# Optimization experiments

Measured on AMD Instinct MI355X. Metric: run time of the kernel, lower is better.

Reference implementation:

```python
import math
import jax, jax.numpy as jnp
import numpy as np

B, L, D, K = 4, 8192, 256, 2
J = math.ceil(math.log((L - 1) / (K - 1) + 1) / math.log(K))  # 13


def setup_inputs() -> dict:
    key = jax.random.key(0)
    ks = jax.random.split(key, 6)
    h_scale = math.sqrt((math.gamma(K / 2) / math.gamma(J + K / 2)) ** (1.0 / J) / 2)
    return {
        "x": jax.random.normal(ks[0], (B, L, D), dtype=jnp.float32),
        "rms_scale": jnp.ones((D,), dtype=jnp.float32),
        "h0": h_scale * jax.random.normal(ks[1], (D, K), dtype=jnp.float32),
        "h1": h_scale * jax.random.normal(ks[2], (D, K), dtype=jnp.float32),
        "w": (1.0 / math.sqrt(J + 2)) * jax.random.normal(ks[3], (J + 2, D), dtype=jnp.float32),
        "conv_w": jax.random.normal(ks[4], (D, 2 * D), dtype=jnp.float32) / math.sqrt(D),
        "conv_b": jnp.zeros((2 * D,), dtype=jnp.float32),
    }


def _dw_conv(a, h, dilation, d):
    # depthwise dilated 1D conv, VALID padding; a: [B, Lpad, D], h: [1, D, K]
    return jax.lax.conv_general_dilated(
        lhs=a, rhs=h, window_strides=(1,), padding='VALID',
        dimension_numbers=('NLC', 'IOL', 'NLC'),
        rhs_dilation=(dilation,), feature_group_count=d)


def reference(x, rms_scale, h0, h1, w, conv_w, conv_b):
    d = x.shape[-1]
    k = h0.shape[-1]
    n_levels = w.shape[0] - 2
    skip = x
    # RMSNorm (flax default eps=1e-6)
    x = x * jax.lax.rsqrt(jnp.mean(jnp.square(x), axis=-1, keepdims=True) + 1e-6) * rms_scale
    # MultiResLayer (pad_right=False -> left pad, causal)
    h0e = h0[None, :, :]  # [1, D, K]
    h1e = h1[None, :, :]
    y = jnp.zeros_like(x)
    a = x
    for j in range(n_levels):
        dilation = k ** j
        pad = dilation * (k - 1)
        a = jnp.pad(a, ((0, 0), (pad, 0), (0, 0)))
        b = _dw_conv(a, h1e, dilation, d)
        a = _dw_conv(a, h0e, dilation, d)
        y = y + w[j + 1][None, None, :] * b
    y = y + w[None, :1, :] * x + w[None, -1:, :] * a
    # activation -> pointwise conv to 2D -> GLU -> residual
    y = jax.nn.gelu(y)  # approximate=True matches flax nn.gelu default
    y = jnp.einsum('bld,de->ble', y, conv_w) + conv_b
    y = jax.nn.glu(y, axis=-1)
    return y + skip
```

## Files before the change

kernel.cpp:

```cpp
#include <hip/hip_runtime.h>
#include <hip/hip_bf16.h>

#define B_ 4
#define L_ 8192
#define D_ 256
#define J_ 13

typedef __attribute__((ext_vector_type(4))) float f32x4;
typedef __attribute__((ext_vector_type(8))) short bf16x8;

__device__ __forceinline__ void async_copy16(const void* g, void* l) {
    __builtin_amdgcn_global_load_lds(
        (const __attribute__((address_space(1))) void*)g,
        (__attribute__((address_space(3))) void*)l, 16, 0, 0);
}

__global__ void wt_kernel(const float* __restrict__ W, __hip_bfloat16* __restrict__ Wt) {
    __shared__ float tile[64][65];
    int blk = blockIdx.x;
    int dt = blk >> 3, et = blk & 7;
    int d0 = dt * 64, e0 = et * 64;
    int tid = threadIdx.x;
#pragma unroll
    for (int k = 0; k < 16; ++k) {
        int i = tid + k * 256;
        int r = i >> 6, c = i & 63;
        tile[r][c] = W[(d0 + r) * 512 + e0 + c];
    }
    __syncthreads();
#pragma unroll
    for (int k = 0; k < 16; ++k) {
        int i = tid + k * 256;
        int r = i >> 6, c = i & 63;
        Wt[(e0 + r) * 256 + d0 + c] = __float2bfloat16(tile[c][r]);
    }
}

__global__ void rms_kernel(const float* __restrict__ x, const float* __restrict__ scale,
                           float* __restrict__ xt) {
    __shared__ float tile[32][257];
    __shared__ float invl[32];
    int blk = blockIdx.x;
    int b  = blk >> 8;
    int l0 = (blk & 255) << 5;
    int tid = threadIdx.x;
    const float* src = x + ((size_t)(b * L_ + l0)) * D_;
#pragma unroll
    for (int k = 0; k < 32; ++k) tile[k][tid] = src[k * D_ + tid];
    __syncthreads();
    int wave = tid >> 6, lane = tid & 63;
#pragma unroll
    for (int rr = 0; rr < 8; ++rr) {
        int r = wave * 8 + rr;
        float s = 0.f;
#pragma unroll
        for (int q = 0; q < 4; ++q) { float v = tile[r][lane + 64 * q]; s += v * v; }
#pragma unroll
        for (int off = 32; off; off >>= 1) s += __shfl_xor(s, off);
        if (lane == 0) invl[r] = rsqrtf(s * (1.0f / 256.0f) + 1e-6f);
    }
    __syncthreads();
#pragma unroll
    for (int k = 0; k < 32; ++k) {
        int i = tid + k * 256;
        int d = i >> 5, lr = i & 31;
        float v = tile[lr][d] * invl[lr] * scale[d];
        xt[((size_t)(b * D_ + d)) * L_ + l0 + lr] = v;
    }
}

__global__ void __launch_bounds__(512, 4) cascade_kernel(
    const float* __restrict__ xt, const float* __restrict__ h0,
    const float* __restrict__ h1, const float* __restrict__ w,
    __hip_bfloat16* __restrict__ ygt) {
    __shared__ float bufA[L_];
    __shared__ float bufB[L_];
    int blk = blockIdx.x;
    int c = blk & 255;
    int tid = threadIdx.x;
    const float4* s4 = (const float4*)(xt + ((size_t)blk) * L_);
    float4* a4 = (float4*)bufA;
#pragma unroll
    for (int q = 0; q < 4; ++q) a4[tid + q * 512] = s4[tid + q * 512];
    float h00 = h0[c * 2], h01 = h0[c * 2 + 1];
    float h10 = h1[c * 2], h11 = h1[c * 2 + 1];
    float w0 = w[c], wlast = w[14 * D_ + c];
    __syncthreads();

    float2 y[8];
    {
        float wj = w[1 * D_ + c];
        const float2* c2 = (const float2*)bufA;
        float2* n2 = (float2*)bufB;
#pragma unroll
        for (int m = 0; m < 8; ++m) {
            int p = tid + m * 512;
            float2 cv = c2[p];
            float px = (p > 0) ? bufA[2 * p - 1] : 0.f;
            float py = cv.x;
            y[m].x = w0 * cv.x + wj * (h10 * px + h11 * cv.x);
            y[m].y = w0 * cv.y + wj * (h10 * py + h11 * cv.y);
            n2[p] = make_float2(h00 * px + h01 * cv.x, h00 * py + h01 * cv.y);
        }
        __syncthreads();
    }
    float* cur = bufB;
    float* nxt = bufA;
#pragma unroll 1
    for (int j = 1; j < J_; ++j) {
        int dh = 1 << (j - 1);
        float wj = w[(j + 1) * D_ + c];
        const float2* c2 = (const float2*)cur;
        float2* n2 = (float2*)nxt;
#pragma unroll
        for (int m = 0; m < 8; ++m) {
            int p = tid + m * 512;
            float2 cv = c2[p];
            int q = p - dh;
            float2 pv = (q >= 0) ? c2[q] : make_float2(0.f, 0.f);
            y[m].x += wj * (h10 * pv.x + h11 * cv.x);
            y[m].y += wj * (h10 * pv.y + h11 * cv.y);
            n2[p] = make_float2(h00 * pv.x + h01 * cv.x, h00 * pv.y + h01 * cv.y);
        }
        __syncthreads();
        float* t = cur; cur = nxt; nxt = t;
    }
    {
        const float2* c2 = (const float2*)cur;
        __hip_bfloat162* o2 = (__hip_bfloat162*)(ygt + ((size_t)blk) * L_);
#pragma unroll
        for (int m = 0; m < 8; ++m) {
            int p = tid + m * 512;
            float2 cv = c2[p];
            float vx = y[m].x + wlast * cv.x;
            float vy = y[m].y + wlast * cv.y;
            float ux = 0.7978845608028654f * (vx + 0.044715f * vx * vx * vx);
            float uy = 0.7978845608028654f * (vy + 0.044715f * vy * vy * vy);
            float gx = 0.5f * vx * (1.f + tanhf(ux));
            float gy = 0.5f * vy * (1.f + tanhf(uy));
            __hip_bfloat162 o;
            o.x = __float2bfloat16(gx);
            o.y = __float2bfloat16(gy);
            o2[p] = o;
        }
    }
}

__global__ void trans_kernel(const ushort* __restrict__ ygt, ushort* __restrict__ yg) {
    __shared__ uint tile[64][33];
    int blk = blockIdx.x;
    int b = blk >> 9;
    int rem = blk & 511;
    int dt = rem >> 7, lt = rem & 127;
    int d0 = dt * 64, l0 = lt * 64;
    int tid = threadIdx.x;
    const uint* src = (const uint*)ygt;
#pragma unroll
    for (int k = 0; k < 8; ++k) {
        int i = tid + k * 256;
        int r = i >> 5, cp = i & 31;
        tile[r][cp] = src[(((size_t)(b * D_ + d0 + r)) * L_ + l0) / 2 + cp];
    }
    __syncthreads();
    const ushort* ts = (const ushort*)tile;
#pragma unroll
    for (int k = 0; k < 16; ++k) {
        int i = tid + k * 256;
        int r2 = i >> 6, c2 = i & 63;
        yg[((size_t)(b * L_ + l0 + r2)) * D_ + d0 + c2] = ts[c2 * 66 + r2];
    }
}

__global__ void __launch_bounds__(256) gemm_kernel(
    const ushort* __restrict__ yg, const ushort* __restrict__ Wt,
    const float* __restrict__ cb, const float* __restrict__ x,
    float* __restrict__ out) {
    __shared__ __align__(16) char smem[32768];
    ushort* As = (ushort*)smem;
    ushort* Bs = As + 128 * 64;
    int blk = blockIdx.x;
    int b = blk >> 8;
    int rem = blk & 255;
    int ltile = rem >> 2, et = rem & 3;
    int l0 = ltile * 128, e0 = et * 64;
    int tid = threadIdx.x;
    int wave = tid >> 6, lane = tid & 63;
    int wm = wave >> 1, wn = wave & 1;
    int m0 = wm * 64;

    int srow_in = (lane >> 3);
    int sg = lane & 7;
    int sgg = sg ^ srow_in;
    f32x4 acc[4][4];
#pragma unroll
    for (int i = 0; i < 4; ++i)
#pragma unroll
        for (int j = 0; j < 4; ++j) acc[i][j] = (f32x4)0.f;

    for (int kc = 0; kc < 4; ++kc) {
        __syncthreads();
#pragma unroll
        for (int v = 0; v < 4; ++v) {
            int r = wave * 32 + v * 8 + srow_in;
            async_copy16(yg + ((size_t)(b * L_ + l0 + r)) * D_ + kc * 64 + sgg * 8,
                         As + r * 64 + sg * 8);
            int e = (r < 64) ? (e0 + r) : (256 + e0 + (r - 64));
            async_copy16(Wt + e * 256 + kc * 64 + sgg * 8,
                         Bs + r * 64 + sg * 8);
        }
        __syncthreads();
#pragma unroll
        for (int kk = 0; kk < 2; ++kk) {
            bf16x8 af[4], bfr[4];
            int g = kk * 4 + (lane >> 4);
            int gp = (g ^ (lane & 7)) * 8;
#pragma unroll
            for (int mt = 0; mt < 4; ++mt)
                af[mt] = *(const bf16x8*)(As + (m0 + mt * 16 + (lane & 15)) * 64 + gp);
#pragma unroll
            for (int nt = 0; nt < 4; ++nt) {
                int n = wn * 32 + (nt & 1) * 16 + (nt >> 1) * 64 + (lane & 15);
                bfr[nt] = *(const bf16x8*)(Bs + n * 64 + gp);
            }
#pragma unroll
            for (int mt = 0; mt < 4; ++mt)
#pragma unroll
                for (int nt = 0; nt < 4; ++nt)
                    acc[mt][nt] = __builtin_amdgcn_mfma_f32_16x16x32_bf16(
                        af[mt], bfr[nt], acc[mt][nt], 0, 0, 0);
        }
    }
    __syncthreads();
    float* epi = (float*)smem;
    int row_in = (lane >> 4) * 4;
    int col = lane & 15;
#pragma unroll
    for (int mt = 0; mt < 4; ++mt) {
#pragma unroll
        for (int p = 0; p < 2; ++p) {
            f32x4 uacc = acc[mt][p];
            f32x4 vacc = acc[mt][p + 2];
            int ee = wn * 32 + p * 16 + col;
            float bu = cb[e0 + ee], bv = cb[256 + e0 + ee];
#pragma unroll
            for (int r = 0; r < 4; ++r) {
                int ll = m0 + mt * 16 + row_in + r;
                float u = uacc[r] + bu;
                float v = vacc[r] + bv;
                float g = u / (1.f + __expf(-v));
                epi[ll * 64 + (ee ^ ((ll & 4) ? 16 : 0))] = g;
            }
        }
    }
    __syncthreads();
#pragma unroll
    for (int k = 0; k < 8; ++k) {
        int i = tid + k * 256;
        int ll = i >> 4, e4 = i & 15;
        int ex = (e4 * 4) ^ ((ll & 4) ? 16 : 0);
        float4 gv = *(const float4*)(epi + ll * 64 + ex);
        size_t gidx = ((size_t)(b * L_ + l0 + ll)) * D_ + e0 + e4 * 4;
        float4 xv = *(const float4*)(x + gidx);
        float4 ov;
        ov.x = gv.x + xv.x; ov.y = gv.y + xv.y;
        ov.z = gv.z + xv.z; ov.w = gv.w + xv.w;
        *(float4*)(out + gidx) = ov;
    }
}

extern "C" void kernel_launch(void* const* d_in, const int* in_sizes, int n_in,
                              void* d_out, int out_size, void* d_ws, size_t ws_size,
                              hipStream_t stream) {
    const float* x  = (const float*)d_in[0];
    const float* rs = (const float*)d_in[1];
    const float* h0 = (const float*)d_in[2];
    const float* h1 = (const float*)d_in[3];
    const float* w  = (const float*)d_in[4];
    const float* cw = (const float*)d_in[5];
    const float* cb = (const float*)d_in[6];
    float* out = (float*)d_out;
    char* ws = (char*)d_ws;

    float*          xt  = (float*)ws;
    __hip_bfloat16* ygt = (__hip_bfloat16*)(ws + 33554432);
    __hip_bfloat16* Wt  = (__hip_bfloat16*)(ws + 50331648);
    ushort*         yg  = (ushort*)ws;

    wt_kernel<<<32, 256, 0, stream>>>(cw, Wt);
    rms_kernel<<<1024, 256, 0, stream>>>(x, rs, xt);
    cascade_kernel<<<1024, 512, 0, stream>>>(xt, h0, h1, w, ygt);
    trans_kernel<<<2048, 256, 0, stream>>>((const ushort*)ygt, yg);
    gemm_kernel<<<1024, 256, 0, stream>>>(yg, (const ushort*)Wt, cb, x, out);
}
```

Before: 163.9 us.

## Keep cascade state in registers with per-thread contiguous chunks and halo exchange

The dilated-conv cascade kernel now gives each thread 16 contiguous sequence elements held in registers, instead of ping-ponging full-length rows between two shared-memory buffers. The first four levels (dilation 1 to 8) read only the previous thread's tail through a small shared exchange buffer. Deeper levels shift whole thread chunks by exchanging them through shared memory. This cuts LDS traffic and size, so launch bounds rise to 6 blocks per CU for occupancy, but it adds an extra barrier per small level and more register pressure.

```diff
diff --git a/kernel.cpp b/kernel.cpp
--- a/kernel.cpp
+++ b/kernel.cpp
@@ -8,6 +8,7 @@
 
 typedef __attribute__((ext_vector_type(4))) float f32x4;
 typedef __attribute__((ext_vector_type(8))) short bf16x8;
+typedef __attribute__((ext_vector_type(8))) unsigned short u16x8;
 
 __device__ __forceinline__ void async_copy16(const void* g, void* l) {
     __builtin_amdgcn_global_load_lds(
@@ -69,81 +70,107 @@
     }
 }
 
-__global__ void __launch_bounds__(512, 4) cascade_kernel(
+#define LEVEL_SMALL(dconst)                                                     \
+    do {                                                                        \
+        *(float4*)&ex[t20 + 8]  = make_float4(cc[8], cc[9], cc[10], cc[11]);    \
+        *(float4*)&ex[t20 + 12] = make_float4(cc[12], cc[13], cc[14], cc[15]);  \
+        __syncthreads();                                                        \
+        float pt[8];                                                            \
+        if (t > 0) {                                                            \
+            float4 p0 = *(const float4*)&ex[t20 - 20 + 8];                      \
+            float4 p1 = *(const float4*)&ex[t20 - 20 + 12];                     \
+            pt[0]=p0.x; pt[1]=p0.y; pt[2]=p0.z; pt[3]=p0.w;                     \
+            pt[4]=p1.x; pt[5]=p1.y; pt[6]=p1.z; pt[7]=p1.w;                     \
+        } else { _Pragma("unroll") for (int i=0;i<8;++i) pt[i]=0.f; }           \
+        __syncthreads();                                                        \
+        float wj = w[((dconst##_J)+1) * D_ + c];                                \
+        _Pragma("unroll")                                                       \
+        for (int i = 15; i >= 0; --i) {                                         \
+            float pv = (i >= (dconst)) ? cc[i - (dconst)] : pt[8 + i - (dconst)]; \
+            float nv = h00 * pv + h01 * cc[i];                                  \
+            y[i] += wj * (h10 * pv + h11 * cc[i]);                              \
+            cc[i] = nv;                                                         \
+        }                                                                       \
+    } while (0)
+#define d1_J 0
+#define d2_J 1
+#define d4_J 2
+#define d8_J 3
+#define d1 1
+#define d2 2
+#define d4 4
+#define d8 8
+
+__global__ void __launch_bounds__(512, 6) cascade_kernel(
     const float* __restrict__ xt, const float* __restrict__ h0,
     const float* __restrict__ h1, const float* __restrict__ w,
     __hip_bfloat16* __restrict__ ygt) {
-    __shared__ float bufA[L_];
-    __shared__ float bufB[L_];
+    __shared__ float ex[512 * 20];
     int blk = blockIdx.x;
     int c = blk & 255;
-    int tid = threadIdx.x;
-    const float4* s4 = (const float4*)(xt + ((size_t)blk) * L_);
-    float4* a4 = (float4*)bufA;
-#pragma unroll
-    for (int q = 0; q < 4; ++q) a4[tid + q * 512] = s4[tid + q * 512];
+    int t = threadIdx.x;
+    int t20 = t * 20;
     float h00 = h0[c * 2], h01 = h0[c * 2 + 1];
     float h10 = h1[c * 2], h11 = h1[c * 2 + 1];
     float w0 = w[c], wlast = w[14 * D_ + c];
-    __syncthreads();
-
-    float2 y[8];
-    {
-        float wj = w[1 * D_ + c];
-        const float2* c2 = (const float2*)bufA;
-        float2* n2 = (float2*)bufB;
-#pragma unroll
-        for (int m = 0; m < 8; ++m) {
-            int p = tid + m * 512;
-            float2 cv = c2[p];
-            float px = (p > 0) ? bufA[2 * p - 1] : 0.f;
-            float py = cv.x;
-            y[m].x = w0 * cv.x + wj * (h10 * px + h11 * cv.x);
-            y[m].y = w0 * cv.y + wj * (h10 * py + h11 * cv.y);
-            n2[p] = make_float2(h00 * px + h01 * cv.x, h00 * py + h01 * cv.y);
-        }
+
+    const float* src = xt + ((size_t)blk) * L_ + t * 16;
+    float cc[16], y[16];
+#pragma unroll
+    for (int m = 0; m < 4; ++m) {
+        float4 v = *(const float4*)(src + 4 * m);
+        cc[4*m+0] = v.x; cc[4*m+1] = v.y; cc[4*m+2] = v.z; cc[4*m+3] = v.w;
+    }
+#pragma unroll
+    for (int i = 0; i < 16; ++i) y[i] = w0 * cc[i];
+
+    LEVEL_SMALL(d1);
+    LEVEL_SMALL(d2);
+    LEVEL_SMALL(d4);
+    LEVEL_SMALL(d8);
+
+#pragma unroll 1
+    for (int j = 4; j < J_; ++j) {
+        int dT = 1 << (j - 4);
+        float wj = w[(j + 1) * D_ + c];
+        *(float4*)&ex[t20 + 0]  = make_float4(cc[0], cc[1], cc[2], cc[3]);
+        *(float4*)&ex[t20 + 4]  = make_float4(cc[4], cc[5], cc[6], cc[7]);
+        *(float4*)&ex[t20 + 8]  = make_float4(cc[8], cc[9], cc[10], cc[11]);
+        *(float4*)&ex[t20 + 12] = make_float4(cc[12], cc[13], cc[14], cc[15]);
         __syncthreads();
-    }
-    float* cur = bufB;
-    float* nxt = bufA;
-#pragma unroll 1
-    for (int j = 1; j < J_; ++j) {
-        int dh = 1 << (j - 1);
-        float wj = w[(j + 1) * D_ + c];
-        const float2* c2 = (const float2*)cur;
-        float2* n2 = (float2*)nxt;
-#pragma unroll
-        for (int m = 0; m < 8; ++m) {
-            int p = tid + m * 512;
-            float2 cv = c2[p];
-            int q = p - dh;
-            float2 pv = (q >= 0) ? c2[q] : make_float2(0.f, 0.f);
-            y[m].x += wj * (h10 * pv.x + h11 * cv.x);
-            y[m].y += wj * (h10 * pv.y + h11 * cv.y);
-            n2[p] = make_float2(h00 * pv.x + h01 * cv.x, h00 * pv.y + h01 * cv.y);
+        float pv[16];
+        if (t >= dT) {
+            int pb = (t - dT) * 20;
+#pragma unroll
+            for (int m = 0; m < 4; ++m) {
+                float4 p = *(const float4*)&ex[pb + 4 * m];
+                pv[4*m+0] = p.x; pv[4*m+1] = p.y; pv[4*m+2] = p.z; pv[4*m+3] = p.w;
+            }
+        } else {
+#pragma unroll
+            for (int i = 0; i < 16; ++i) pv[i] = 0.f;
         }
         __syncthreads();
-        float* t = cur; cur = nxt; nxt = t;
-    }
-    {
-        const float2* c2 = (const float2*)cur;
-        __hip_bfloat162* o2 = (__hip_bfloat162*)(ygt + ((size_t)blk) * L_);
-#pragma unroll
-        for (int m = 0; m < 8; ++m) {
-            int p = tid + m * 512;
-            float2 cv = c2[p];
-            float vx = y[m].x + wlast * cv.x;
-            float vy = y[m].y + wlast * cv.y;
-            float ux = 0.7978845608028654f * (vx + 0.044715f * vx * vx * vx);
-            float uy = 0.7978845608028654f * (vy + 0.044715f * vy * vy * vy);
-            float gx = 0.5f * vx * (1.f + tanhf(ux));
-            float gy = 0.5f * vy * (1.f + tanhf(uy));
-            __hip_bfloat162 o;
-            o.x = __float2bfloat16(gx);
-            o.y = __float2bfloat16(gy);
-            o2[p] = o;
-        }
-    }
+#pragma unroll
+        for (int i = 0; i < 16; ++i) {
+            float nv = h00 * pv[i] + h01 * cc[i];
+            y[i] += wj * (h10 * pv[i] + h11 * cc[i]);
+            cc[i] = nv;
+        }
+    }
+    u16x8 o0, o1;
+#pragma unroll
+    for (int i = 0; i < 16; ++i) {
+        float v = y[i] + wlast * cc[i];
+        float u = 0.7978845608028654f * (v + 0.044715f * v * v * v);
+        float g = 0.5f * v * (1.f + tanhf(u));
+        union { __hip_bfloat16 b; unsigned short us; } cvt;
+        cvt.b = __float2bfloat16(g);
+        if (i < 8) o0[i] = cvt.us; else o1[i - 8] = cvt.us;
+    }
+    unsigned short* dst = (unsigned short*)(ygt + ((size_t)blk) * L_ + t * 16);
+    *(u16x8*)dst = o0;
+    *(u16x8*)(dst + 8) = o1;
 }
 
 __global__ void trans_kernel(const ushort* __restrict__ ygt, ushort* __restrict__ yg) {
```

Result: slower. 167.2 us (+2.1%).

## Register-resident cascade with bf16 intermediate and fused RMS/weight-transpose launch

Applied to the files above, without the earlier changes.

The cascade kernel now keeps 32 consecutive positions per thread in registers and handles two channels per block. Only boundary values are exchanged through a small LDS buffer stored as bf16, so the full-sequence fp32 ping-pong buffers are gone. The RMSNorm output is written as bf16 instead of fp32, halving that intermediate's traffic, and the weight-transpose kernel is folded into the RMS launch. The changes cut LDS footprint, global bandwidth and one launch, at the cost of bf16 rounding of the cascade state at every level, which may affect accuracy.

```diff
diff --git a/kernel.cpp b/kernel.cpp
--- a/kernel.cpp
+++ b/kernel.cpp
@@ -8,6 +8,7 @@
 
 typedef __attribute__((ext_vector_type(4))) float f32x4;
 typedef __attribute__((ext_vector_type(8))) short bf16x8;
+typedef __attribute__((ext_vector_type(8))) unsigned short u16x8;
 
 __device__ __forceinline__ void async_copy16(const void* g, void* l) {
     __builtin_amdgcn_global_load_lds(
@@ -15,35 +16,45 @@
         (__attribute__((address_space(3))) void*)l, 16, 0, 0);
 }
 
-__global__ void wt_kernel(const float* __restrict__ W, __hip_bfloat16* __restrict__ Wt) {
-    __shared__ float tile[64][65];
+__device__ __forceinline__ unsigned int packbf(float a, float b) {
+    unsigned int ua = __float_as_uint(a) + 0x8000u;
+    unsigned int ub = __float_as_uint(b) + 0x8000u;
+    return (ua >> 16) | (ub & 0xFFFF0000u);
+}
+__device__ __forceinline__ unsigned short packbf1(float a) {
+    return (unsigned short)((__float_as_uint(a) + 0x8000u) >> 16);
+}
+
+__global__ void rms_wt_kernel(const float* __restrict__ x, const float* __restrict__ scale,
+                              ushort* __restrict__ xtb,
+                              const float* __restrict__ W, ushort* __restrict__ Wt) {
+    __shared__ __align__(16) float sm[32 * 257 + 32];
     int blk = blockIdx.x;
-    int dt = blk >> 3, et = blk & 7;
-    int d0 = dt * 64, e0 = et * 64;
     int tid = threadIdx.x;
-#pragma unroll
-    for (int k = 0; k < 16; ++k) {
-        int i = tid + k * 256;
-        int r = i >> 6, c = i & 63;
-        tile[r][c] = W[(d0 + r) * 512 + e0 + c];
-    }
-    __syncthreads();
-#pragma unroll
-    for (int k = 0; k < 16; ++k) {
-        int i = tid + k * 256;
-        int r = i >> 6, c = i & 63;
-        Wt[(e0 + r) * 256 + d0 + c] = __float2bfloat16(tile[c][r]);
-    }
-}
-
-__global__ void rms_kernel(const float* __restrict__ x, const float* __restrict__ scale,
-                           float* __restrict__ xt) {
-    __shared__ float tile[32][257];
-    __shared__ float invl[32];
-    int blk = blockIdx.x;
+    if (blk < 32) {
+        float (*tile)[65] = (float(*)[65])sm;
+        int dt = blk >> 3, et = blk & 7;
+        int d0 = dt * 64, e0 = et * 64;
+#pragma unroll
+        for (int k = 0; k < 16; ++k) {
+            int i = tid + k * 256;
+            int r = i >> 6, c = i & 63;
+            tile[r][c] = W[(d0 + r) * 512 + e0 + c];
+        }
+        __syncthreads();
+#pragma unroll
+        for (int k = 0; k < 16; ++k) {
+            int i = tid + k * 256;
+            int r = i >> 6, c = i & 63;
+            Wt[(e0 + r) * 256 + d0 + c] = packbf1(tile[c][r]);
+        }
+        return;
+    }
+    blk -= 32;
+    float (*tile)[257] = (float(*)[257])sm;
+    float* invl = sm + 32 * 257;
     int b  = blk >> 8;
     int l0 = (blk & 255) << 5;
-    int tid = threadIdx.x;
     const float* src = x + ((size_t)(b * L_ + l0)) * D_;
 #pragma unroll
     for (int k = 0; k < 32; ++k) tile[k][tid] = src[k * D_ + tid];
@@ -60,89 +71,134 @@
         if (lane == 0) invl[r] = rsqrtf(s * (1.0f / 256.0f) + 1e-6f);
     }
     __syncthreads();
-#pragma unroll
-    for (int k = 0; k < 32; ++k) {
+    uint* dst32 = (uint*)xtb;
+#pragma unroll
+    for (int k = 0; k < 16; ++k) {
         int i = tid + k * 256;
-        int d = i >> 5, lr = i & 31;
-        float v = tile[lr][d] * invl[lr] * scale[d];
-        xt[((size_t)(b * D_ + d)) * L_ + l0 + lr] = v;
-    }
-}
+        int d = i >> 4, lp = (i & 15) * 2;
+        float v0 = tile[lp][d]     * invl[lp]     * scale[d];
+        float v1 = tile[lp + 1][d] * invl[lp + 1] * scale[d];
+        dst32[(((size_t)(b * D_ + d)) * L_ + l0 + lp) >> 1] = packbf(v0, v1);
+    }
+}
+
+#define LEVEL_SMALL(d, jj)                                                       \
+    do {                                                                         \
+        uint4 pk;                                                                \
+        pk.x = packbf(cc[16], cc[17]); pk.y = packbf(cc[18], cc[19]);            \
+        pk.z = packbf(cc[20], cc[21]); pk.w = packbf(cc[22], cc[23]);            \
+        *(uint4*)(ex + slot + 16) = pk;                                          \
+        pk.x = packbf(cc[24], cc[25]); pk.y = packbf(cc[26], cc[27]);            \
+        pk.z = packbf(cc[28], cc[29]); pk.w = packbf(cc[30], cc[31]);            \
+        *(uint4*)(ex + slot + 24) = pk;                                          \
+        __syncthreads();                                                         \
+        float pt[16];                                                            \
+        if (ct > 0) {                                                            \
+            uint4 a  = *(const uint4*)(ex + slot - 40 + 16);                     \
+            uint4 bq = *(const uint4*)(ex + slot - 40 + 24);                     \
+            uint uu[8] = {a.x, a.y, a.z, a.w, bq.x, bq.y, bq.z, bq.w};           \
+            _Pragma("unroll") for (int q = 0; q < 8; ++q) {                      \
+                pt[2*q]   = __uint_as_float(uu[q] << 16);                        \
+                pt[2*q+1] = __uint_as_float(uu[q] & 0xFFFF0000u); }              \
+        } else { _Pragma("unroll") for (int q = 0; q < 16; ++q) pt[q] = 0.f; }   \
+        __syncthreads();                                                         \
+        float wj = w[((jj) + 1) * D_ + c];                                       \
+        _Pragma("unroll")                                                        \
+        for (int i = 31; i >= 0; --i) {                                          \
+            float pv = (i >= (d)) ? cc[i - (d)] : pt[16 + i - (d)];              \
+            float nv = h00 * pv + h01 * cc[i];                                   \
+            y[i] += wj * (h10 * pv + h11 * cc[i]);                               \
+            cc[i] = nv;                                                          \
+        }                                                                        \
+    } while (0)
 
 __global__ void __launch_bounds__(512, 4) cascade_kernel(
-    const float* __restrict__ xt, const float* __restrict__ h0,
+    const ushort* __restrict__ xt, const float* __restrict__ h0,
     const float* __restrict__ h1, const float* __restrict__ w,
-    __hip_bfloat16* __restrict__ ygt) {
-    __shared__ float bufA[L_];
-    __shared__ float bufB[L_];
+    ushort* __restrict__ ygt) {
+    __shared__ __align__(16) ushort ex[512 * 40];
     int blk = blockIdx.x;
-    int c = blk & 255;
-    int tid = threadIdx.x;
-    const float4* s4 = (const float4*)(xt + ((size_t)blk) * L_);
-    float4* a4 = (float4*)bufA;
-#pragma unroll
-    for (int q = 0; q < 4; ++q) a4[tid + q * 512] = s4[tid + q * 512];
-    float h00 = h0[c * 2], h01 = h0[c * 2 + 1];
-    float h10 = h1[c * 2], h11 = h1[c * 2 + 1];
+    int b = blk >> 7;
+    int t = threadIdx.x;
+    int ch = t >> 8;
+    int ct = t & 255;
+    int c = ((blk & 127) << 1) + ch;
+    int slot = t * 40;
+    float h00 = h0[2*c], h01 = h0[2*c+1];
+    float h10 = h1[2*c], h11 = h1[2*c+1];
     float w0 = w[c], wlast = w[14 * D_ + c];
-    __syncthreads();
-
-    float2 y[8];
-    {
-        float wj = w[1 * D_ + c];
-        const float2* c2 = (const float2*)bufA;
-        float2* n2 = (float2*)bufB;
-#pragma unroll
-        for (int m = 0; m < 8; ++m) {
-            int p = tid + m * 512;
-            float2 cv = c2[p];
-            float px = (p > 0) ? bufA[2 * p - 1] : 0.f;
-            float py = cv.x;
-            y[m].x = w0 * cv.x + wj * (h10 * px + h11 * cv.x);
-            y[m].y = w0 * cv.y + wj * (h10 * py + h11 * cv.y);
-            n2[p] = make_float2(h00 * px + h01 * cv.x, h00 * py + h01 * cv.y);
-        }
-        __syncthreads();
-    }
-    float* cur = bufB;
-    float* nxt = bufA;
+
+    const ushort* src = xt + ((size_t)(b * D_ + c)) * L_ + ct * 32;
+    float cc[32], y[32];
+#pragma unroll
+    for (int m = 0; m < 4; ++m) {
+        u16x8 v = *(const u16x8*)(src + m * 8);
+#pragma unroll
+        for (int i = 0; i < 8; ++i) cc[m*8+i] = __uint_as_float(((uint)v[i]) << 16);
+    }
+#pragma unroll
+    for (int i = 0; i < 32; ++i) y[i] = w0 * cc[i];
+
+    LEVEL_SMALL(1, 0);
+    LEVEL_SMALL(2, 1);
+    LEVEL_SMALL(4, 2);
+    LEVEL_SMALL(8, 3);
+    LEVEL_SMALL(16, 4);
+
 #pragma unroll 1
-    for (int j = 1; j < J_; ++j) {
-        int dh = 1 << (j - 1);
+    for (int j = 5; j < J_; ++j) {
+        int dT = 1 << (j - 5);
         float wj = w[(j + 1) * D_ + c];
-        const float2* c2 = (const float2*)cur;
-        float2* n2 = (float2*)nxt;
-#pragma unroll
-        for (int m = 0; m < 8; ++m) {
-            int p = tid + m * 512;
-            float2 cv = c2[p];
-            int q = p - dh;
-            float2 pv = (q >= 0) ? c2[q] : make_float2(0.f, 0.f);
-            y[m].x += wj * (h10 * pv.x + h11 * cv.x);
-            y[m].y += wj * (h10 * pv.y + h11 * cv.y);
-            n2[p] = make_float2(h00 * pv.x + h01 * cv.x, h00 * pv.y + h01 * cv.y);
-        }
-        __syncthreads();
-        float* t = cur; cur = nxt; nxt = t;
-    }
-    {
-        const float2* c2 = (const float2*)cur;
-        __hip_bfloat162* o2 = (__hip_bfloat162*)(ygt + ((size_t)blk) * L_);
-#pragma unroll
-        for (int m = 0; m < 8; ++m) {
-            int p = tid + m * 512;
-            float2 cv = c2[p];
-            float vx = y[m].x + wlast * cv.x;
-            float vy = y[m].y + wlast * cv.y;
-            float ux = 0.7978845608028654f * (vx + 0.044715f * vx * vx * vx);
-            float uy = 0.7978845608028654f * (vy + 0.044715f * vy * vy * vy);
-            float gx = 0.5f * vx * (1.f + tanhf(ux));
-            float gy = 0.5f * vy * (1.f + tanhf(uy));
-            __hip_bfloat162 o;
-            o.x = __float2bfloat16(gx);
-            o.y = __float2bfloat16(gy);
-            o2[p] = o;
-        }
+#pragma unroll
+        for (int m = 0; m < 4; ++m) {
+            uint4 pk;
+            pk.x = packbf(cc[8*m],   cc[8*m+1]); pk.y = packbf(cc[8*m+2], cc[8*m+3]);
+            pk.z = packbf(cc[8*m+4], cc[8*m+5]); pk.w = packbf(cc[8*m+6], cc[8*m+7]);
+            *(uint4*)(ex + slot + 8 * m) = pk;
+        }
+        __syncthreads();
+        bool has = (ct >= dT);
+        int pbase = slot - dT * 40;
+#pragma unroll
+        for (int h = 0; h < 2; ++h) {
+            float pv[16];
+            if (has) {
+                uint4 a  = *(const uint4*)(ex + pbase + 16 * h);
+                uint4 bq = *(const uint4*)(ex + pbase + 16 * h + 8);
+                uint uu[8] = {a.x, a.y, a.z, a.w, bq.x, bq.y, bq.z, bq.w};
+#pragma unroll
+                for (int q = 0; q < 8; ++q) {
+                    pv[2*q]   = __uint_as_float(uu[q] << 16);
+                    pv[2*q+1] = __uint_as_float(uu[q] & 0xFFFF0000u);
+                }
+            } else {
+#pragma unroll
+                for (int q = 0; q < 16; ++q) pv[q] = 0.f;
+            }
+#pragma unroll
+            for (int i = 0; i < 16; ++i) {
+                int e = 16 * h + i;
+                float nv = h00 * pv[i] + h01 * cc[e];
+                y[e] += wj * (h10 * pv[i] + h11 * cc[e]);
+                cc[e] = nv;
+            }
+        }
+        __syncthreads();
+    }
+    ushort* dst = ygt + ((size_t)(b * D_ + c)) * L_ + ct * 32;
+#pragma unroll
+    for (int m = 0; m < 4; ++m) {
+        float g[8];
+#pragma unroll
+        for (int q = 0; q < 8; ++q) {
+            float v = y[8*m+q] + wlast * cc[8*m+q];
+            float u = 0.7978845608028654f * (v + 0.044715f * v * v * v);
+            g[q] = 0.5f * v * (1.f + tanhf(u));
+        }
+        uint4 pk;
+        pk.x = packbf(g[0], g[1]); pk.y = packbf(g[2], g[3]);
+        pk.z = packbf(g[4], g[5]); pk.w = packbf(g[6], g[7]);
+        *(uint4*)(dst + 8 * m) = pk;
     }
 }
 
@@ -257,8 +313,8 @@
     for (int k = 0; k < 8; ++k) {
         int i = tid + k * 256;
         int ll = i >> 4, e4 = i & 15;
-        int ex = (e4 * 4) ^ ((ll & 4) ? 16 : 0);
-        float4 gv = *(const float4*)(epi + ll * 64 + ex);
+        int exo = (e4 * 4) ^ ((ll & 4) ? 16 : 0);
+        float4 gv = *(const float4*)(epi + ll * 64 + exo);
         size_t gidx = ((size_t)(b * L_ + l0 + ll)) * D_ + e0 + e4 * 4;
         float4 xv = *(const float4*)(x + gidx);
         float4 ov;
@@ -281,14 +337,13 @@
     float* out = (float*)d_out;
     char* ws = (char*)d_ws;
 
-    float*          xt  = (float*)ws;
-    __hip_bfloat16* ygt = (__hip_bfloat16*)(ws + 33554432);
-    __hip_bfloat16* Wt  = (__hip_bfloat16*)(ws + 50331648);
-    ushort*         yg  = (ushort*)ws;
-
-    wt_kernel<<<32, 256, 0, stream>>>(cw, Wt);
-    rms_kernel<<<1024, 256, 0, stream>>>(x, rs, xt);
-    cascade_kernel<<<1024, 512, 0, stream>>>(xt, h0, h1, w, ygt);
-    trans_kernel<<<2048, 256, 0, stream>>>((const ushort*)ygt, yg);
-    gemm_kernel<<<1024, 256, 0, stream>>>(yg, (const ushort*)Wt, cb, x, out);
-}
+    ushort* xtb = (ushort*)ws;
+    ushort* ygt = (ushort*)(ws + 16777216);
+    ushort* Wt  = (ushort*)(ws + 33554432);
+    ushort* yg  = (ushort*)ws;
+
+    rms_wt_kernel<<<1056, 256, 0, stream>>>(x, rs, xtb, cw, Wt);
+    cascade_kernel<<<512, 512, 0, stream>>>(xtb, h0, h1, w, ygt);
+    trans_kernel<<<2048, 256, 0, stream>>>(ygt, yg);
+    gemm_kernel<<<1024, 256, 0, stream>>>(yg, Wt, cb, x, out);
+}
```

After: 208.7 us. 27.4% more time.
